# Kernel optimization log

Hardware: AMD Instinct MI355X
Metric: run time of the kernel (lower is better)

## Reference

```python
import jax, jax.numpy as jnp
import numpy as np

N_NODES = 100000
N_EDGES = 1600000
IN_FEATS = 128
HIDDEN = 128
OUT_FEATS = 40


def glorot(key, out_dim, in_dim):
    lim = np.sqrt(6.0 / (in_dim + out_dim)).astype(np.float32)
    return jax.random.uniform(key, (out_dim, in_dim), jnp.float32, -lim, lim)


def setup_inputs() -> dict:
    key = jax.random.key(0)
    ks = jax.random.split(key, 10)
    x = jax.random.normal(ks[0], (N_NODES, IN_FEATS), jnp.float32)
    edge_index = jax.random.randint(ks[1], (2, N_EDGES), 0, N_NODES, jnp.int32)
    return {
        "x": x,
        "edge_index": edge_index,
        # SAGEConv1: lin_l (on aggregated neighbors, with bias), lin_r (root, no bias)
        "W1_l": glorot(ks[2], HIDDEN, IN_FEATS),
        "b1": jnp.zeros((HIDDEN,), jnp.float32),
        "W1_r": glorot(ks[3], HIDDEN, IN_FEATS),
        # SAGEConv2
        "W2_l": glorot(ks[4], HIDDEN, HIDDEN),
        "b2": jnp.zeros((HIDDEN,), jnp.float32),
        "W2_r": glorot(ks[5], HIDDEN, HIDDEN),
        # classifier Linear
        "Wc": glorot(ks[6], OUT_FEATS, HIDDEN),
        "bc": jnp.zeros((OUT_FEATS,), jnp.float32),
    }


def _sage_conv(x, src, dst, W_l, b_l, W_r):
    # PyG SAGEConv with mean aggregation:
    # out = lin_l(mean_{j in N(i)} x_j) + lin_r(x_i)
    msg = x[src]                                   # [E, F] gather
    agg = jax.ops.segment_sum(msg, dst, num_segments=N_NODES)   # [N, F] scatter-add
    deg = jax.ops.segment_sum(jnp.ones((src.shape[0], 1), x.dtype), dst,
                              num_segments=N_NODES)             # [N, 1]
    agg = agg / jnp.maximum(deg, 1.0)
    return agg @ W_l.T + b_l + x @ W_r.T


def reference(x, edge_index, W1_l, b1, W1_r, W2_l, b2, W2_r, Wc, bc):
    src, dst = edge_index[0], edge_index[1]
    # dropout is identity in eval mode
    h = _sage_conv(x, src, dst, W1_l, b1, W1_r)
    h = jax.nn.relu(h)
    h = _sage_conv(h, src, dst, W2_l, b2, W2_r)
    embedding = h
    logits = embedding @ Wc.T + bc
    soft_label = jax.nn.softmax(logits, axis=1)
    hard_label = jnp.argmax(soft_label, axis=1)
    return logits, embedding, soft_label, hard_label
```

## Files before the change

kernel.cpp:

```cpp
#include <hip/hip_runtime.h>


#define FEATS 128
#define SCAN_CHUNK 4096
#define BSHIFT 9
#define BSIZE  (1 << BSHIFT)
#define MAXNB  256
#define EPB    8192

static __device__ __forceinline__ float4 ld4(const float* p) {
    return *reinterpret_cast<const float4*>(p);
}


__global__ __launch_bounds__(256)
void hist_kernel(const int* __restrict__ dst, int* __restrict__ bhist,
                 int E, int NB, int nblkA) {
    __shared__ int hist[MAXNB];
    const int tid = threadIdx.x, blk = blockIdx.x;
    for (int t = tid; t < MAXNB; t += 256) hist[t] = 0;
    __syncthreads();
    const int e0 = blk * EPB;
    const int e1 = min(E, e0 + EPB);
    for (int i = e0 + tid; i < e1; i += 256)
        atomicAdd(&hist[dst[i] >> BSHIFT], 1);
    __syncthreads();
    for (int t = tid; t < NB; t += 256) bhist[t * nblkA + blk] = hist[t];
}

__global__ __launch_bounds__(256)
void scan_partial(const int* __restrict__ cnt, int* __restrict__ part, int N) {
    __shared__ int red[256];
    const int base = blockIdx.x * SCAN_CHUNK;
    int sum = 0;
    for (int i = threadIdx.x; i < SCAN_CHUNK; i += 256) {
        int idx = base + i;
        sum += (idx < N) ? cnt[idx] : 0;
    }
    red[threadIdx.x] = sum;
    __syncthreads();
    for (int off = 128; off > 0; off >>= 1) {
        if (threadIdx.x < off) red[threadIdx.x] += red[threadIdx.x + off];
        __syncthreads();
    }
    if (threadIdx.x == 0) part[blockIdx.x] = red[0];
}

__global__ __launch_bounds__(1024)
void scan_part2(int* __restrict__ part, int nb, int* __restrict__ totalp) {
    __shared__ int s[1024];
    const int tid = threadIdx.x;
    s[tid] = (tid < nb) ? part[tid] : 0;
    __syncthreads();
    for (int off = 1; off < 1024; off <<= 1) {
        int t = (tid >= off) ? s[tid - off] : 0;
        __syncthreads();
        s[tid] += t;
        __syncthreads();
    }
    if (tid < nb) part[tid] = (tid == 0) ? 0 : s[tid - 1];
    if (tid == 0) *totalp = s[1023];
}

__global__ __launch_bounds__(256)
void scan_out(const int* __restrict__ cnt, const int* __restrict__ part,
              int* __restrict__ out, int Ntot) {
    __shared__ int tsum[256];
    const int tid = threadIdx.x;
    const int myb = blockIdx.x * SCAN_CHUNK + tid * 16;
    int v[16];
    int s = 0;
    #pragma unroll
    for (int j = 0; j < 16; j++) {
        int idx = myb + j;
        int c = (idx < Ntot) ? cnt[idx] : 0;
        v[j] = s; s += c;
    }
    tsum[tid] = s;
    __syncthreads();
    for (int off = 1; off < 256; off <<= 1) {
        int t = (tid >= off) ? tsum[tid - off] : 0;
        __syncthreads();
        tsum[tid] += t;
        __syncthreads();
    }
    const int base = part[blockIdx.x] + ((tid == 0) ? 0 : tsum[tid - 1]);
    #pragma unroll
    for (int j = 0; j < 16; j++) {
        int idx = myb + j;
        if (idx < Ntot) out[idx] = base + v[j];
    }
}

__global__ __launch_bounds__(256)
void scatter_kernel(const int* __restrict__ src, const int* __restrict__ dst,
                    const int* __restrict__ scanT, int* __restrict__ packed,
                    int E, int NB, int nblkA) {
    __shared__ int cur[MAXNB];
    const int tid = threadIdx.x, blk = blockIdx.x;
    for (int t = tid; t < NB; t += 256) cur[t] = scanT[t * nblkA + blk];
    __syncthreads();
    const int e0 = blk * EPB;
    const int e1 = min(E, e0 + EPB);
    for (int i = e0 + tid; i < e1; i += 256) {
        int d = dst[i], s = src[i];
        int bkt = d >> BSHIFT;
        int slot = atomicAdd(&cur[bkt], 1);
        packed[slot] = ((d & (BSIZE - 1)) << 17) | s;
    }
}

__global__ __launch_bounds__(256)
void bucket_csr(const int* __restrict__ packed, const int* __restrict__ scanT,
                int* __restrict__ offs, int* __restrict__ ssrc,
                int N, int E, int NB, int nblkA) {
    __shared__ int lcnt[BSIZE];
    __shared__ int lofs[BSIZE];
    __shared__ int s[256];
    const int tid = threadIdx.x, b = blockIdx.x;
    const int base_b = scanT[b * nblkA];
    const int end_b = (b == NB - 1) ? E : scanT[(b + 1) * nblkA];
    const int n0 = b << BSHIFT;
    const int nn = min(BSIZE, N - n0);

    lcnt[tid] = 0; lcnt[tid + 256] = 0;
    __syncthreads();
    for (int i = base_b + tid; i < end_b; i += 256)
        atomicAdd(&lcnt[packed[i] >> 17], 1);
    __syncthreads();

    const int a0 = lcnt[2 * tid], a1 = lcnt[2 * tid + 1];
    s[tid] = a0 + a1;
    __syncthreads();
    for (int off = 1; off < 256; off <<= 1) {
        int t = (tid >= off) ? s[tid - off] : 0;
        __syncthreads();
        s[tid] += t;
        __syncthreads();
    }
    const int ebase = (tid == 0) ? 0 : s[tid - 1];
    lofs[2 * tid] = ebase;
    lofs[2 * tid + 1] = ebase + a0;
    __syncthreads();

    for (int j = tid; j < nn; j += 256) offs[n0 + j] = base_b + lofs[j];
    if (b == NB - 1 && tid == 0) offs[N] = E;
    __syncthreads();

    for (int i = base_b + tid; i < end_b; i += 256) {
        int c = packed[i];
        int slot = atomicAdd(&lofs[c >> 17], 1);
        ssrc[base_b + slot] = c & 0x1FFFF;
    }
}

__global__ __launch_bounds__(256)
void agg_kernel(const float2* __restrict__ x2, const int* __restrict__ ssrc,
                const int* __restrict__ offs, float2* __restrict__ out2, int N) {
    const int g = blockIdx.x * 4 + (threadIdx.x >> 6);
    const int lane = threadIdx.x & 63;
    if (g >= N) return;
    const int beg = offs[g], end = offs[g + 1];
    float ax = 0.f, ay = 0.f;
    int e = beg;
    for (; e + 1 < end; e += 2) {
        int s0 = ssrc[e], s1 = ssrc[e + 1];
        float2 v0 = x2[(size_t)s0 * 64 + lane];
        float2 v1 = x2[(size_t)s1 * 64 + lane];
        ax += v0.x + v1.x; ay += v0.y + v1.y;
    }
    if (e < end) {
        int s0 = ssrc[e];
        float2 v0 = x2[(size_t)s0 * 64 + lane];
        ax += v0.x; ay += v0.y;
    }
    const int d = end - beg;
    const float inv = 1.0f / (float)(d > 1 ? d : 1);
    float2 o; o.x = ax * inv; o.y = ay * inv;
    out2[(size_t)g * 64 + lane] = o;
}

__global__ __launch_bounds__(256)
void sage_gemm(const float* __restrict__ A1, const float* __restrict__ A2,
               const float* __restrict__ Wl, const float* __restrict__ Wr,
               const float* __restrict__ bias, float* __restrict__ C,
               int M, int do_relu) {
    __shared__ float As[16][132];
    __shared__ float Bs[16][132];
    const int tid = threadIdx.x;
    const int tr = tid >> 4;
    const int tc = tid & 15;
    const int row0 = blockIdx.x * 128;
    const int lr = tid >> 2;
    const int lk = (tid & 3) << 2;
    const int bcol = tid >> 1;
    const int bkq = (tid & 1) << 3;

    float acc[8][8];
    #pragma unroll
    for (int m = 0; m < 8; m++)
        #pragma unroll
        for (int n = 0; n < 8; n++) acc[m][n] = 0.f;

    for (int kk = 0; kk < 16; kk++) {
        const float* Asrc = (kk < 8) ? A1 : A2;
        const float* Wsrc = (kk < 8) ? Wl : Wr;
        const int k0 = (kk & 7) << 4;

        #pragma unroll
        for (int h = 0; h < 2; h++) {
            const int r = lr + h * 64;
            const int gr = row0 + r;
            float4 av = make_float4(0.f, 0.f, 0.f, 0.f);
            if (gr < M) av = ld4(Asrc + (size_t)gr * FEATS + k0 + lk);
            As[lk + 0][r] = av.x; As[lk + 1][r] = av.y;
            As[lk + 2][r] = av.z; As[lk + 3][r] = av.w;
        }

        float4 b0 = ld4(Wsrc + (size_t)bcol * FEATS + k0 + bkq);
        float4 b1 = ld4(Wsrc + (size_t)bcol * FEATS + k0 + bkq + 4);
        Bs[bkq + 0][bcol] = b0.x; Bs[bkq + 1][bcol] = b0.y;
        Bs[bkq + 2][bcol] = b0.z; Bs[bkq + 3][bcol] = b0.w;
        Bs[bkq + 4][bcol] = b1.x; Bs[bkq + 5][bcol] = b1.y;
        Bs[bkq + 6][bcol] = b1.z; Bs[bkq + 7][bcol] = b1.w;
        __syncthreads();

        #pragma unroll
        for (int k = 0; k < 16; k++) {
            float4 a0 = *(const float4*)&As[k][tr * 8];
            float4 a1 = *(const float4*)&As[k][tr * 8 + 4];
            float4 b0v = *(const float4*)&Bs[k][tc * 8];
            float4 b1v = *(const float4*)&Bs[k][tc * 8 + 4];
            float am[8] = {a0.x, a0.y, a0.z, a0.w, a1.x, a1.y, a1.z, a1.w};
            float bn[8] = {b0v.x, b0v.y, b0v.z, b0v.w, b1v.x, b1v.y, b1v.z, b1v.w};
            #pragma unroll
            for (int m = 0; m < 8; m++)
                #pragma unroll
                for (int n = 0; n < 8; n++)
                    acc[m][n] += am[m] * bn[n];
        }
        __syncthreads();
    }

    float4 bv0 = ld4(bias + tc * 8);
    float4 bv1 = ld4(bias + tc * 8 + 4);
    float bb[8] = {bv0.x, bv0.y, bv0.z, bv0.w, bv1.x, bv1.y, bv1.z, bv1.w};
    #pragma unroll
    for (int m = 0; m < 8; m++) {
        const int r = row0 + tr * 8 + m;
        if (r < M) {
            float o[8];
            #pragma unroll
            for (int n = 0; n < 8; n++) {
                o[n] = acc[m][n] + bb[n];
                if (do_relu) o[n] = fmaxf(o[n], 0.f);
            }
            float* cp = C + (size_t)r * FEATS + tc * 8;
            *reinterpret_cast<float4*>(cp)     = make_float4(o[0], o[1], o[2], o[3]);
            *reinterpret_cast<float4*>(cp + 4) = make_float4(o[4], o[5], o[6], o[7]);
        }
    }
}

__global__ __launch_bounds__(256)
void classifier_kernel(const float* __restrict__ emb, const float* __restrict__ Wc,
                       const float* __restrict__ bc, float* __restrict__ logits,
                       float* __restrict__ soft, float* __restrict__ hard, int N) {
    __shared__ float Ws[40 * 128];
    __shared__ float bs[40];
    for (int i = threadIdx.x; i < 40 * 128; i += 256) Ws[i] = Wc[i];
    if (threadIdx.x < 40) bs[threadIdx.x] = bc[threadIdx.x];
    __syncthreads();
    const int row = blockIdx.x * 256 + threadIdx.x;
    if (row >= N) return;

    float acc[40];
    #pragma unroll
    for (int f = 0; f < 40; f++) acc[f] = 0.f;

    const float* erow = emb + (size_t)row * FEATS;
    for (int c = 0; c < 8; c++) {
        float4 r0 = ld4(erow + c * 16 + 0);
        float4 r1 = ld4(erow + c * 16 + 4);
        float4 r2 = ld4(erow + c * 16 + 8);
        float4 r3 = ld4(erow + c * 16 + 12);
        #pragma unroll
        for (int f = 0; f < 40; f++) {
            const float* w = &Ws[f * 128 + c * 16];
            float4 w0 = ld4(w), w1 = ld4(w + 4), w2 = ld4(w + 8), w3 = ld4(w + 12);
            acc[f] += r0.x * w0.x + r0.y * w0.y + r0.z * w0.z + r0.w * w0.w
                    + r1.x * w1.x + r1.y * w1.y + r1.z * w1.z + r1.w * w1.w
                    + r2.x * w2.x + r2.y * w2.y + r2.z * w2.z + r2.w * w2.w
                    + r3.x * w3.x + r3.y * w3.y + r3.z * w3.z + r3.w * w3.w;
        }
    }
    #pragma unroll
    for (int f = 0; f < 40; f++) acc[f] += bs[f];

    float m = acc[0]; int idx = 0;
    #pragma unroll
    for (int f = 1; f < 40; f++) { if (acc[f] > m) { m = acc[f]; idx = f; } }

    float* lrow = logits + (size_t)row * 40;
    #pragma unroll
    for (int f = 0; f < 40; f++) lrow[f] = acc[f];

    float sum = 0.f;
    #pragma unroll
    for (int f = 0; f < 40; f++) { acc[f] = __expf(acc[f] - m); sum += acc[f]; }
    const float inv = 1.0f / sum;
    float* srow = soft + (size_t)row * 40;
    #pragma unroll
    for (int f = 0; f < 40; f++) srow[f] = acc[f] * inv;
    hard[row] = (float)idx;
}


static inline size_t align16(size_t x) { return (x + 15) & ~(size_t)15; }

extern "C" void kernel_launch(void* const* d_in, const int* in_sizes, int n_in,
                              void* d_out, int out_size, void* d_ws, size_t ws_size,
                              hipStream_t stream) {
    const float* x   = (const float*)d_in[0];
    const int*   ei  = (const int*)d_in[1];
    const float* W1l = (const float*)d_in[2];
    const float* b1  = (const float*)d_in[3];
    const float* W1r = (const float*)d_in[4];
    const float* W2l = (const float*)d_in[5];
    const float* b2  = (const float*)d_in[6];
    const float* W2r = (const float*)d_in[7];
    const float* Wc  = (const float*)d_in[8];
    const float* bc  = (const float*)d_in[9];

    const int N = in_sizes[0] / FEATS;
    const int E = in_sizes[1] / 2;
    const int* src = ei;
    const int* dst = ei + E;

    const int NB    = (N + BSIZE - 1) >> BSHIFT;
    const int nblkA = (E + EPB - 1) / EPB;
    const int T     = NB * nblkA;
    const int nb2   = (T + SCAN_CHUNK - 1) / SCAN_CHUNK;

    char* ws = (char*)d_ws;
    size_t oScanT = 0;
    size_t oBhist = oScanT + align16((size_t)(T + 1) * 4);
    size_t oPart  = oBhist + align16((size_t)T * 4);
    size_t oOffs  = oPart  + align16((size_t)1024 * 4);
    size_t oSsrc  = oOffs  + align16((size_t)(N + 1) * 4);
    size_t oAgg   = oSsrc  + align16((size_t)E * 4);
    int*   scanT  = (int*)(ws + oScanT);
    int*   bhist  = (int*)(ws + oBhist);
    int*   part   = (int*)(ws + oPart);
    int*   offs   = (int*)(ws + oOffs);
    int*   ssrc   = (int*)(ws + oSsrc);
    float* aggbuf = (float*)(ws + oAgg);
    int*   packed = (int*)(ws + oAgg);

    float* out    = (float*)d_out;
    float* logits = out;
    float* emb    = out + (size_t)N * 40;
    float* soft   = emb + (size_t)N * FEATS;
    float* hard   = soft + (size_t)N * 40;

    const int gridAgg = (N + 3) / 4;
    const int gridGemm = (N + 127) / 128;
    const int gridRow = (N + 255) / 256;

    hist_kernel<<<nblkA, 256, 0, stream>>>(dst, bhist, E, NB, nblkA);
    scan_partial<<<nb2, 256, 0, stream>>>(bhist, part, T);
    scan_part2<<<1, 1024, 0, stream>>>(part, nb2, scanT + T);
    scan_out<<<nb2, 256, 0, stream>>>(bhist, part, scanT, T);
    scatter_kernel<<<nblkA, 256, 0, stream>>>(src, dst, scanT, packed, E, NB, nblkA);
    bucket_csr<<<NB, 256, 0, stream>>>(packed, scanT, offs, ssrc, N, E, NB, nblkA);

    agg_kernel<<<gridAgg, 256, 0, stream>>>((const float2*)x, ssrc, offs, (float2*)aggbuf, N);
    sage_gemm<<<gridGemm, 256, 0, stream>>>(aggbuf, x, W1l, W1r, b1, emb, N, 1);

    agg_kernel<<<gridAgg, 256, 0, stream>>>((const float2*)emb, ssrc, offs, (float2*)aggbuf, N);
    sage_gemm<<<gridGemm, 256, 0, stream>>>(aggbuf, emb, W2l, W2r, b2, emb, N, 0);

    classifier_kernel<<<gridRow, 256, 0, stream>>>(emb, Wc, bc, logits, soft, hard, N);
}
```

Before: 697.7 us.

## Split neighbor aggregation into two feature-half passes with edge-parallel half-waves

```diff
diff --git a/kernel.cpp b/kernel.cpp
--- a/kernel.cpp
+++ b/kernel.cpp
@@ -155,29 +155,42 @@
 }
 
 __global__ __launch_bounds__(256)
-void agg_kernel(const float2* __restrict__ x2, const int* __restrict__ ssrc,
-                const int* __restrict__ offs, float2* __restrict__ out2, int N) {
+void agg_half(const float2* __restrict__ x2, const int* __restrict__ ssrc,
+              const int* __restrict__ offs, float2* __restrict__ out2,
+              int N, int half) {
     const int g = blockIdx.x * 4 + (threadIdx.x >> 6);
     const int lane = threadIdx.x & 63;
+    const int h = lane >> 5, li = lane & 31;
     if (g >= N) return;
+    const int hoff = half * 32;
     const int beg = offs[g], end = offs[g + 1];
     float ax = 0.f, ay = 0.f;
     int e = beg;
-    for (; e + 1 < end; e += 2) {
-        int s0 = ssrc[e], s1 = ssrc[e + 1];
-        float2 v0 = x2[(size_t)s0 * 64 + lane];
-        float2 v1 = x2[(size_t)s1 * 64 + lane];
-        ax += v0.x + v1.x; ay += v0.y + v1.y;
-    }
-    if (e < end) {
-        int s0 = ssrc[e];
-        float2 v0 = x2[(size_t)s0 * 64 + lane];
-        ax += v0.x; ay += v0.y;
-    }
+    for (; e + 4 <= end; e += 4) {
+        int sA = ssrc[e + h];
+        int sB = ssrc[e + 2 + h];
+        float2 vA = x2[(size_t)sA * 64 + hoff + li];
+        float2 vB = x2[(size_t)sB * 64 + hoff + li];
+        ax += vA.x + vB.x;
+        ay += vA.y + vB.y;
+    }
+    for (; e + 2 <= end; e += 2) {
+        int sA = ssrc[e + h];
+        float2 v = x2[(size_t)sA * 64 + hoff + li];
+        ax += v.x; ay += v.y;
+    }
+    if (e < end && h == 0) {
+        float2 v = x2[(size_t)ssrc[e] * 64 + hoff + li];
+        ax += v.x; ay += v.y;
+    }
+    ax += __shfl_xor(ax, 32, 64);
+    ay += __shfl_xor(ay, 32, 64);
     const int d = end - beg;
     const float inv = 1.0f / (float)(d > 1 ? d : 1);
-    float2 o; o.x = ax * inv; o.y = ay * inv;
-    out2[(size_t)g * 64 + lane] = o;
+    if (h == 0) {
+        float2 o; o.x = ax * inv; o.y = ay * inv;
+        out2[(size_t)g * 64 + hoff + li] = o;
+    }
 }
 
 __global__ __launch_bounds__(256)
@@ -208,8 +221,8 @@
         const int k0 = (kk & 7) << 4;
 
         #pragma unroll
-        for (int h = 0; h < 2; h++) {
-            const int r = lr + h * 64;
+        for (int hh = 0; hh < 2; hh++) {
+            const int r = lr + hh * 64;
             const int gr = row0 + r;
             float4 av = make_float4(0.f, 0.f, 0.f, 0.f);
             if (gr < M) av = ld4(Asrc + (size_t)gr * FEATS + k0 + lk);
@@ -349,13 +362,13 @@
     size_t oOffs  = oPart  + align16((size_t)1024 * 4);
     size_t oSsrc  = oOffs  + align16((size_t)(N + 1) * 4);
     size_t oAgg   = oSsrc  + align16((size_t)E * 4);
-    int*   scanT  = (int*)(ws + oScanT);
-    int*   bhist  = (int*)(ws + oBhist);
-    int*   part   = (int*)(ws + oPart);
-    int*   offs   = (int*)(ws + oOffs);
-    int*   ssrc   = (int*)(ws + oSsrc);
-    float* aggbuf = (float*)(ws + oAgg);
-    int*   packed = (int*)(ws + oAgg);
+    int*    scanT = (int*)(ws + oScanT);
+    int*    bhist = (int*)(ws + oBhist);
+    int*    part  = (int*)(ws + oPart);
+    int*    offs  = (int*)(ws + oOffs);
+    int*    ssrc  = (int*)(ws + oSsrc);
+    float*  aggbuf = (float*)(ws + oAgg);
+    int*    packed = (int*)(ws + oAgg);
 
     float* out    = (float*)d_out;
     float* logits = out;
@@ -363,9 +376,9 @@
     float* soft   = emb + (size_t)N * FEATS;
     float* hard   = soft + (size_t)N * 40;
 
-    const int gridAgg = (N + 3) / 4;
+    const int gridAgg  = (N + 3) / 4;
     const int gridGemm = (N + 127) / 128;
-    const int gridRow = (N + 255) / 256;
+    const int gridRow  = (N + 255) / 256;
 
     hist_kernel<<<nblkA, 256, 0, stream>>>(dst, bhist, E, NB, nblkA);
     scan_partial<<<nb2, 256, 0, stream>>>(bhist, part, T);
@@ -374,10 +387,16 @@
     scatter_kernel<<<nblkA, 256, 0, stream>>>(src, dst, scanT, packed, E, NB, nblkA);
     bucket_csr<<<NB, 256, 0, stream>>>(packed, scanT, offs, ssrc, N, E, NB, nblkA);
 
-    agg_kernel<<<gridAgg, 256, 0, stream>>>((const float2*)x, ssrc, offs, (float2*)aggbuf, N);
+    agg_half<<<gridAgg, 256, 0, stream>>>((const float2*)x, ssrc, offs,
+                                          (float2*)aggbuf, N, 0);
+    agg_half<<<gridAgg, 256, 0, stream>>>((const float2*)x, ssrc, offs,
+                                          (float2*)aggbuf, N, 1);
     sage_gemm<<<gridGemm, 256, 0, stream>>>(aggbuf, x, W1l, W1r, b1, emb, N, 1);
 
-    agg_kernel<<<gridAgg, 256, 0, stream>>>((const float2*)emb, ssrc, offs, (float2*)aggbuf, N);
+    agg_half<<<gridAgg, 256, 0, stream>>>((const float2*)emb, ssrc, offs,
+                                          (float2*)aggbuf, N, 0);
+    agg_half<<<gridAgg, 256, 0, stream>>>((const float2*)emb, ssrc, offs,
+                                          (float2*)aggbuf, N, 1);
     sage_gemm<<<gridGemm, 256, 0, stream>>>(aggbuf, emb, W2l, W2r, b2, emb, N, 0);
 
     classifier_kernel<<<gridRow, 256, 0, stream>>>(emb, Wc, bc, logits, soft, hard, N);
```

After: 729.0 us. 1.04x slower.
